# Optimization experiments

Hardware: AMD Instinct MI355X
Metric: run time of the kernel (lower is better)

## Reference

```python
import jax, jax.numpy as jnp
import numpy as np

B, S, K, V, H = 32, 2048, 512, 512, 256


def setup_inputs() -> dict:
    key = jax.random.key(0)
    ks = jax.random.split(key, 6)
    r = 0.1  # init_range
    return {
        "q": jax.random.normal(ks[0], (B, K), jnp.float32),
        "k": jax.random.normal(ks[1], (S, B, K), jnp.float32),
        "v": jax.random.normal(ks[2], (S, B, V), jnp.float32),
        "Wk": jax.random.uniform(ks[3], (H, K), jnp.float32, -r, r),
        "bk": jnp.zeros((H,), jnp.float32),
        "Wq": jax.random.uniform(ks[4], (H, K), jnp.float32, -r, r),
        "bq": jnp.zeros((H,), jnp.float32),
        "Wo": jax.random.uniform(ks[5], (1, H), jnp.float32, -r, r),
        "bo": jnp.zeros((1,), jnp.float32),
    }


def reference(q, k, v, Wk, bk, Wq, bq, Wo, bo):
    # k, v: [S, B, *] -> batch-first [B, S, *]
    kb = jnp.transpose(k, (1, 0, 2))  # [B, S, K]
    vb = jnp.transpose(v, (1, 0, 2))  # [B, S, V]
    h_k = jnp.einsum('bsk,hk->bsh', kb, Wk) + bk        # key2hid
    h_q = q @ Wq.T + bq                                  # [B, H]
    h = jnp.tanh(h_k + h_q[:, None, :])                  # [B, S, H]
    logit = jnp.einsum('bsh,h->bs', h, Wo[0]) + bo[0]    # hid2output, squeeze
    logit = logit - jnp.max(logit, axis=1, keepdims=True)
    p = jax.nn.softmax(logit, axis=1)                    # [B, S]
    out = jnp.sum(vb * p[:, :, None], axis=1, keepdims=True)  # [B, 1, V]
    out = jnp.transpose(out, (1, 0, 2))                  # [1, B, V]
    return out, p
```

## Files before the change

kernel.cpp:

```cpp
#include <hip/hip_runtime.h>
#include <stdint.h>

#define Bb 32
#define Ss 2048
#define Kk 512
#define Vv 512
#define Hh 256

#define OUTP (Bb * Vv)

#define WS_HQ 0
#define WS_WKB 32768
#define WS_LOGIT 294912

typedef float floatx4 __attribute__((ext_vector_type(4)));
typedef __bf16 bf16x8 __attribute__((ext_vector_type(8)));

__device__ __forceinline__ uint32_t bfround(float f) {
  uint32_t u = __float_as_uint(f);
  return (u + 0x7fffu + ((u >> 16) & 1u)) >> 16;
}
__device__ __forceinline__ uint32_t packbf(float lo, float hi) {
  return bfround(lo) | (bfround(hi) << 16);
}

__device__ __forceinline__ void gload_lds16(const uint16_t* g, uint16_t* l) {
  __builtin_amdgcn_global_load_lds((const __attribute__((address_space(1))) void*)g,
                                   (__attribute__((address_space(3))) void*)l, 16, 0, 0);
}

__global__ void prep(const float* __restrict__ q, const float* __restrict__ Wq,
                     const float* __restrict__ bq, const float* __restrict__ bk,
                     const float* __restrict__ Wk, uint16_t* __restrict__ wkb,
                     float* __restrict__ hq) {
  __shared__ float red[256];
  const int bx = blockIdx.x;
  const int t = threadIdx.x;
  if (bx < 128) {
    const int i = (bx * 256 + t) * 4;
    float4 w = *(const float4*)(Wk + i);
    const int h = i >> 9;
    const int k = i & 511;
    const int stage = k >> 6;
    const int kin = k & 63;
    const int grp = kin >> 3;
    const int j = kin & 7;
    uint2 pk;
    pk.x = packbf(w.x, w.y);
    pk.y = packbf(w.z, w.w);
    *(uint2*)(wkb + stage * 16384 + (grp * 256 + h) * 8 + j) = pk;
  } else {
    const int idx = bx - 128;
    const int b = idx >> 3;
    const int hc = idx & 7;
    const int h_in = t & 31;
    const int kp = t >> 5;
    const int h = hc * 32 + h_in;
    const float4* qp = (const float4*)(q + b * Kk + kp * 64);
    const float4* wp = (const float4*)(Wq + h * Kk + kp * 64);
    float acc = 0.f;
#pragma unroll
    for (int i = 0; i < 16; ++i) {
      float4 qa = qp[i], wa = wp[i];
      acc = fmaf(qa.x, wa.x, acc);
      acc = fmaf(qa.y, wa.y, acc);
      acc = fmaf(qa.z, wa.z, acc);
      acc = fmaf(qa.w, wa.w, acc);
    }
    red[t] = acc;
    __syncthreads();
    if (t < 32) {
      float s = 0.f;
#pragma unroll
      for (int kp2 = 0; kp2 < 8; ++kp2) s += red[kp2 * 32 + t];
      const int hh = hc * 32 + t;
      hq[b * Hh + hh] = s + bq[hh] + bk[hh];
    }
  }
}

__global__ __launch_bounds__(256, 3) void fused_gemm_tanh_logit(
    const float* __restrict__ kin, const uint16_t* __restrict__ wkb,
    const float* __restrict__ hq, const float* __restrict__ Wo,
    float* __restrict__ logits) {
  __shared__ __align__(16) uint16_t lA[64 * 64];
  __shared__ __align__(16) uint16_t lB[256 * 64];
  __shared__ float lpart[4][64];

  const int tid = threadIdx.x;
  const int b = blockIdx.y;
  const int s0 = blockIdx.x * 64;
  const int wid = tid >> 6;
  const int lane = tid & 63;
  const int l15 = lane & 15;
  const int lg = lane >> 4;

  float hqv[4], wov[4];
#pragma unroll
  for (int ni = 0; ni < 4; ++ni) {
    const int n = wid * 64 + ni * 16 + l15;
    hqv[ni] = hq[b * Hh + n];
    wov[ni] = Wo[n];
  }

  floatx4 acc[4][4];
#pragma unroll
  for (int mi = 0; mi < 4; ++mi)
#pragma unroll
    for (int ni = 0; ni < 4; ++ni) acc[mi][ni] = (floatx4){0.f, 0.f, 0.f, 0.f};

  const int kg = tid >> 5;
  const int mrow = (tid & 31) * 2;
  const float* a0 = kin + ((size_t)(s0 + mrow) * Bb + b) * Kk + kg * 8;
  const float* a1 = a0 + (size_t)Bb * Kk;

  float4 av0, av1, av2, av3;
  av0 = *(const float4*)(a0);
  av1 = *(const float4*)(a0 + 4);
  av2 = *(const float4*)(a1);
  av3 = *(const float4*)(a1 + 4);

  const uint16_t* bstage = wkb + (wid * 8) * 512 + lane * 8;
  uint16_t* bdst0 = &lB[(wid * 8) * 512];

  for (int ks = 0; ks < 8; ++ks) {
    __syncthreads();
    uint4 w0, w1;
    w0.x = packbf(av0.x, av0.y);
    w0.y = packbf(av0.z, av0.w);
    w0.z = packbf(av1.x, av1.y);
    w0.w = packbf(av1.z, av1.w);
    w1.x = packbf(av2.x, av2.y);
    w1.y = packbf(av2.z, av2.w);
    w1.z = packbf(av3.x, av3.y);
    w1.w = packbf(av3.z, av3.w);
    *(uint4*)&lA[(kg * 64 + mrow) * 8] = w0;
    *(uint4*)&lA[(kg * 64 + mrow + 1) * 8] = w1;
    const uint16_t* bsrc = bstage + ks * 16384;
#pragma unroll
    for (int it = 0; it < 8; ++it) gload_lds16(bsrc + it * 512, bdst0 + it * 512);
    __syncthreads();
    if (ks < 7) {
      av0 = *(const float4*)(a0 + (ks + 1) * 64);
      av1 = *(const float4*)(a0 + (ks + 1) * 64 + 4);
      av2 = *(const float4*)(a1 + (ks + 1) * 64);
      av3 = *(const float4*)(a1 + (ks + 1) * 64 + 4);
    }
#pragma unroll
    for (int kk = 0; kk < 2; ++kk) {
      bf16x8 af[4], bfr[4];
#pragma unroll
      for (int mi = 0; mi < 4; ++mi)
        af[mi] = *(const bf16x8*)&lA[((kk * 4 + lg) * 64 + mi * 16 + l15) * 8];
#pragma unroll
      for (int ni = 0; ni < 4; ++ni)
        bfr[ni] = *(const bf16x8*)&lB[((kk * 4 + lg) * 256 + wid * 64 + ni * 16 + l15) * 8];
#pragma unroll
      for (int mi = 0; mi < 4; ++mi)
#pragma unroll
        for (int ni = 0; ni < 4; ++ni)
          acc[mi][ni] =
              __builtin_amdgcn_mfma_f32_16x16x32_bf16(af[mi], bfr[ni], acc[mi][ni], 0, 0, 0);
    }
  }

#pragma unroll
  for (int mi = 0; mi < 4; ++mi) {
#pragma unroll
    for (int r = 0; r < 4; ++r) {
      float sum = 0.f;
#pragma unroll
      for (int ni = 0; ni < 4; ++ni) {
        const float x = acc[mi][ni][r] + hqv[ni];
        const float e = __expf(2.f * x);
        const float th = 1.f - 2.f * __builtin_amdgcn_rcpf(e + 1.f);
        sum = fmaf(th, wov[ni], sum);
      }
      sum += __shfl_xor(sum, 1, 64);
      sum += __shfl_xor(sum, 2, 64);
      sum += __shfl_xor(sum, 4, 64);
      sum += __shfl_xor(sum, 8, 64);
      if (l15 == 0) lpart[wid][mi * 16 + lg * 4 + r] = sum;
    }
  }
  __syncthreads();
  if (tid < 64) {
    const float lv = lpart[0][tid] + lpart[1][tid] + lpart[2][tid] + lpart[3][tid];
    logits[b * Ss + s0 + tid] = lv;
  }
}

__global__ void softmax_zero(const float* __restrict__ logits, float* __restrict__ dout) {
  const int b = blockIdx.x;
  const int t = threadIdx.x;
  const int wid = t >> 6, lane = t & 63;
  __shared__ float red[4];
  const float4* lp = (const float4*)(logits + b * Ss);
  const float4 x0 = lp[t * 2], x1 = lp[t * 2 + 1];
  float mx = fmaxf(fmaxf(fmaxf(x0.x, x0.y), fmaxf(x0.z, x0.w)),
                   fmaxf(fmaxf(x1.x, x1.y), fmaxf(x1.z, x1.w)));
#pragma unroll
  for (int off = 1; off < 64; off <<= 1) mx = fmaxf(mx, __shfl_xor(mx, off, 64));
  if (lane == 0) red[wid] = mx;
  __syncthreads();
  mx = fmaxf(fmaxf(red[0], red[1]), fmaxf(red[2], red[3]));
  __syncthreads();
  float e[8];
  e[0] = __expf(x0.x - mx); e[1] = __expf(x0.y - mx);
  e[2] = __expf(x0.z - mx); e[3] = __expf(x0.w - mx);
  e[4] = __expf(x1.x - mx); e[5] = __expf(x1.y - mx);
  e[6] = __expf(x1.z - mx); e[7] = __expf(x1.w - mx);
  float s = ((e[0] + e[1]) + (e[2] + e[3])) + ((e[4] + e[5]) + (e[6] + e[7]));
#pragma unroll
  for (int off = 1; off < 64; off <<= 1) s += __shfl_xor(s, off, 64);
  if (lane == 0) red[wid] = s;
  __syncthreads();
  s = (red[0] + red[1]) + (red[2] + red[3]);
  const float inv = 1.f / s;
  float4 p0, p1;
  p0.x = e[0] * inv; p0.y = e[1] * inv; p0.z = e[2] * inv; p0.w = e[3] * inv;
  p1.x = e[4] * inv; p1.y = e[5] * inv; p1.z = e[6] * inv; p1.w = e[7] * inv;
  float4* pout = (float4*)(dout + OUTP + b * Ss);
  pout[t * 2] = p0;
  pout[t * 2 + 1] = p1;
  dout[b * Vv + t] = 0.f;
  dout[b * Vv + 256 + t] = 0.f;
}

__global__ __launch_bounds__(256) void weighted_vsum(const float* __restrict__ v,
                                                     float* __restrict__ dout) {
  const int sc = blockIdx.x;
  const int b = blockIdx.y;
  const int t = threadIdx.x;
  __shared__ float lp[128];
  if (t < 128) lp[t] = dout[OUTP + b * Ss + sc * 128 + t];
  __syncthreads();
  const int c4 = t & 127;
  const int sh = t >> 7;
  float4 acc = {0.f, 0.f, 0.f, 0.f};
#pragma unroll 8
  for (int i = 0; i < 64; ++i) {
    const int sl = sh + 2 * i;
    const int s = sc * 128 + sl;
    const float4 vv = *(const float4*)(v + ((size_t)s * Bb + b) * Vv + c4 * 4);
    const float pw = lp[sl];
    acc.x = fmaf(pw, vv.x, acc.x);
    acc.y = fmaf(pw, vv.y, acc.y);
    acc.z = fmaf(pw, vv.z, acc.z);
    acc.w = fmaf(pw, vv.w, acc.w);
  }
  float* o = dout + b * Vv + c4 * 4;
  atomicAdd(o + 0, acc.x);
  atomicAdd(o + 1, acc.y);
  atomicAdd(o + 2, acc.z);
  atomicAdd(o + 3, acc.w);
}

extern "C" void kernel_launch(void* const* d_in, const int* in_sizes, int n_in,
                              void* d_out, int out_size, void* d_ws, size_t ws_size,
                              hipStream_t stream) {
  const float* q  = (const float*)d_in[0];
  const float* k  = (const float*)d_in[1];
  const float* v  = (const float*)d_in[2];
  const float* Wk = (const float*)d_in[3];
  const float* bk = (const float*)d_in[4];
  const float* Wq = (const float*)d_in[5];
  const float* bq = (const float*)d_in[6];
  const float* Wo = (const float*)d_in[7];

  float* out = (float*)d_out;
  char* ws = (char*)d_ws;
  float* hq = (float*)(ws + WS_HQ);
  uint16_t* wkb = (uint16_t*)(ws + WS_WKB);
  float* logits = (float*)(ws + WS_LOGIT);

  prep<<<dim3(384), dim3(256), 0, stream>>>(q, Wq, bq, bk, Wk, wkb, hq);
  fused_gemm_tanh_logit<<<dim3(Ss / 64, Bb), dim3(256), 0, stream>>>(k, wkb, hq, Wo, logits);
  softmax_zero<<<dim3(Bb), dim3(256), 0, stream>>>(logits, out);
  weighted_vsum<<<dim3(16, Bb), dim3(256), 0, stream>>>(v, out);
}
```

Baseline: 329.8 us.

## Double-buffer A tile in LDS and load Wk fragments directly into registers

The GEMM main loop now keeps two LDS buffers for the bf16-converted key tile and prefetches the key data two stages ahead. Each wave reads its Wk fragments straight from global memory into registers, double-buffered, so the shared B tile and the global-to-LDS copies are gone. This removes one barrier per stage and lets loads overlap the MFMAs. The price is many more live registers, so occupancy drops from 3 to 2 workgroups per SIMD in the launch bounds, and each wave now fetches B from global or L2 on its own.

```diff
diff --git a/kernel.cpp b/kernel.cpp
--- a/kernel.cpp
+++ b/kernel.cpp
@@ -22,11 +22,6 @@
 }
 __device__ __forceinline__ uint32_t packbf(float lo, float hi) {
   return bfround(lo) | (bfround(hi) << 16);
-}
-
-__device__ __forceinline__ void gload_lds16(const uint16_t* g, uint16_t* l) {
-  __builtin_amdgcn_global_load_lds((const __attribute__((address_space(1))) void*)g,
-                                   (__attribute__((address_space(3))) void*)l, 16, 0, 0);
 }
 
 __global__ void prep(const float* __restrict__ q, const float* __restrict__ Wq,
@@ -79,12 +74,11 @@
   }
 }
 
-__global__ __launch_bounds__(256, 3) void fused_gemm_tanh_logit(
+__global__ __launch_bounds__(256, 2) void fused_gemm_tanh_logit(
     const float* __restrict__ kin, const uint16_t* __restrict__ wkb,
     const float* __restrict__ hq, const float* __restrict__ Wo,
     float* __restrict__ logits) {
-  __shared__ __align__(16) uint16_t lA[64 * 64];
-  __shared__ __align__(16) uint16_t lB[256 * 64];
+  __shared__ __align__(16) uint16_t lA[2][64 * 64];
   __shared__ float lpart[4][64];
 
   const int tid = threadIdx.x;
@@ -109,59 +103,74 @@
 #pragma unroll
     for (int ni = 0; ni < 4; ++ni) acc[mi][ni] = (floatx4){0.f, 0.f, 0.f, 0.f};
 
-  const int kg = tid >> 5;
-  const int mrow = (tid & 31) * 2;
-  const float* a0 = kin + ((size_t)(s0 + mrow) * Bb + b) * Kk + kg * 8;
-  const float* a1 = a0 + (size_t)Bb * Kk;
-
-  float4 av0, av1, av2, av3;
-  av0 = *(const float4*)(a0);
-  av1 = *(const float4*)(a0 + 4);
-  av2 = *(const float4*)(a1);
-  av3 = *(const float4*)(a1 + 4);
-
-  const uint16_t* bstage = wkb + (wid * 8) * 512 + lane * 8;
-  uint16_t* bdst0 = &lB[(wid * 8) * 512];
-
+  const int r0 = tid >> 4;
+  const int j = tid & 15;
+  const size_t CROW = (size_t)16 * Bb * Kk;
+  const float* aptr = kin + ((size_t)(s0 + r0) * Bb + b) * Kk + j * 4;
+  uint16_t* wbase = &lA[0][0] + (((j >> 1) * 64 + r0) * 8 + (j & 1) * 4);
+
+  const uint16_t* bptr = wkb + ((size_t)lg * 256 + wid * 64 + l15) * 8;
+
+  float4 av[4];
+  bf16x8 breg[2][8];
+
+#pragma unroll
+  for (int kk = 0; kk < 2; ++kk)
+#pragma unroll
+    for (int ni = 0; ni < 4; ++ni)
+      breg[0][kk * 4 + ni] = *(const bf16x8*)(bptr + kk * 8192 + ni * 128);
+#pragma unroll
+  for (int c = 0; c < 4; ++c) av[c] = *(const float4*)(aptr + c * CROW);
+#pragma unroll
+  for (int c = 0; c < 4; ++c) {
+    uint2 pk;
+    pk.x = packbf(av[c].x, av[c].y);
+    pk.y = packbf(av[c].z, av[c].w);
+    *(uint2*)(wbase + c * 128) = pk;
+  }
+#pragma unroll
+  for (int c = 0; c < 4; ++c) av[c] = *(const float4*)(aptr + c * CROW + 64);
+  __syncthreads();
+
+#pragma unroll
   for (int ks = 0; ks < 8; ++ks) {
-    __syncthreads();
-    uint4 w0, w1;
-    w0.x = packbf(av0.x, av0.y);
-    w0.y = packbf(av0.z, av0.w);
-    w0.z = packbf(av1.x, av1.y);
-    w0.w = packbf(av1.z, av1.w);
-    w1.x = packbf(av2.x, av2.y);
-    w1.y = packbf(av2.z, av2.w);
-    w1.z = packbf(av3.x, av3.y);
-    w1.w = packbf(av3.z, av3.w);
-    *(uint4*)&lA[(kg * 64 + mrow) * 8] = w0;
-    *(uint4*)&lA[(kg * 64 + mrow + 1) * 8] = w1;
-    const uint16_t* bsrc = bstage + ks * 16384;
-#pragma unroll
-    for (int it = 0; it < 8; ++it) gload_lds16(bsrc + it * 512, bdst0 + it * 512);
-    __syncthreads();
+    const int cur = ks & 1, nxt = cur ^ 1;
     if (ks < 7) {
-      av0 = *(const float4*)(a0 + (ks + 1) * 64);
-      av1 = *(const float4*)(a0 + (ks + 1) * 64 + 4);
-      av2 = *(const float4*)(a1 + (ks + 1) * 64);
-      av3 = *(const float4*)(a1 + (ks + 1) * 64 + 4);
+#pragma unroll
+      for (int kk = 0; kk < 2; ++kk)
+#pragma unroll
+        for (int ni = 0; ni < 4; ++ni)
+          breg[nxt][kk * 4 + ni] =
+              *(const bf16x8*)(bptr + (size_t)(ks + 1) * 16384 + kk * 8192 + ni * 128);
+    }
+    if (ks < 7) {
+#pragma unroll
+      for (int c = 0; c < 4; ++c) {
+        uint2 pk;
+        pk.x = packbf(av[c].x, av[c].y);
+        pk.y = packbf(av[c].z, av[c].w);
+        *(uint2*)(wbase + nxt * 4096 + c * 128) = pk;
+      }
+    }
+    if (ks < 6) {
+#pragma unroll
+      for (int c = 0; c < 4; ++c)
+        av[c] = *(const float4*)(aptr + c * CROW + (ks + 2) * 64);
     }
 #pragma unroll
     for (int kk = 0; kk < 2; ++kk) {
-      bf16x8 af[4], bfr[4];
+      bf16x8 af[4];
 #pragma unroll
       for (int mi = 0; mi < 4; ++mi)
-        af[mi] = *(const bf16x8*)&lA[((kk * 4 + lg) * 64 + mi * 16 + l15) * 8];
-#pragma unroll
-      for (int ni = 0; ni < 4; ++ni)
-        bfr[ni] = *(const bf16x8*)&lB[((kk * 4 + lg) * 256 + wid * 64 + ni * 16 + l15) * 8];
+        af[mi] = *(const bf16x8*)&lA[cur][((kk * 4 + lg) * 64 + mi * 16 + l15) * 8];
 #pragma unroll
       for (int mi = 0; mi < 4; ++mi)
 #pragma unroll
         for (int ni = 0; ni < 4; ++ni)
-          acc[mi][ni] =
-              __builtin_amdgcn_mfma_f32_16x16x32_bf16(af[mi], bfr[ni], acc[mi][ni], 0, 0, 0);
-    }
+          acc[mi][ni] = __builtin_amdgcn_mfma_f32_16x16x32_bf16(
+              af[mi], breg[cur][kk * 4 + ni], acc[mi][ni], 0, 0, 0);
+    }
+    if (ks < 7) __syncthreads();
   }
 
 #pragma unroll
```

After: 318.2 us. 1.04x faster.
